# Kernel optimization log

Hardware: AMD Instinct MI355X
Metric: run time of the kernel (lower is better)

## Reference

```python
import jax, jax.numpy as jnp
import numpy as np

BN_EPS = 1e-5


def setup_inputs() -> dict:
    key = jax.random.key(0)
    k1, k2, k3, k4 = jax.random.split(key, 4)
    N, E, D_IN, D_OUT = 100000, 1600000, 128, 128
    x = jax.random.normal(k1, (N, D_IN), dtype=jnp.float32)
    edge_index = jax.random.randint(k2, (2, E), 0, N, dtype=jnp.int64)
    # GCNConv linear (glorot) + bias (zeros init in PyG)
    W = jax.random.normal(k3, (D_OUT, D_IN), dtype=jnp.float32) * (1.0 / np.sqrt(D_IN))
    b = jnp.zeros((D_OUT,), dtype=jnp.float32)
    # BatchNorm affine params
    gamma = jnp.ones((D_OUT,), dtype=jnp.float32)
    beta = jnp.zeros((D_OUT,), dtype=jnp.float32)
    return {"x": x, "edge_index": edge_index, "W": W, "b": b,
            "gamma": gamma, "beta": beta}


def reference(x, edge_index, W, b, gamma, beta):
    N = x.shape[0]
    # --- GCNConv: add self-loops, symmetric normalization ---
    loop = jnp.arange(N, dtype=edge_index.dtype)
    src = jnp.concatenate([edge_index[0], loop])  # [E+N]
    dst = jnp.concatenate([edge_index[1], loop])  # [E+N]
    deg = jax.ops.segment_sum(jnp.ones_like(dst, dtype=x.dtype), dst,
                              num_segments=N)  # in-degree incl. self-loop
    dinv = jnp.where(deg > 0, jax.lax.rsqrt(deg), 0.0)
    norm = dinv[src] * dinv[dst]  # [E+N]
    # linear transform before propagation (PyG GCNConv)
    h = x @ W.T  # [N, D_OUT]
    agg = jax.ops.segment_sum(h[src] * norm[:, None], dst, num_segments=N)
    out = agg + b
    # --- BatchNorm1d (training mode: batch statistics over nodes) ---
    mean = jnp.mean(out, axis=0)
    var = jnp.var(out, axis=0)
    out = (out - mean) * jax.lax.rsqrt(var + BN_EPS) * gamma + beta
    # --- ReLU, residual, dropout(p=0 -> identity) ---
    out = jax.nn.relu(out)
    out = out + x  # residual (in_dim == out_dim)
    return out
```

## Files before the change

### kernel.cpp

```cpp
#include <hip/hip_runtime.h>
#include <hip/hip_fp16.h>

#define BN_EPS 1e-5f

typedef unsigned int uint32;
typedef __attribute__((ext_vector_type(8))) _Float16 f16x8;
typedef __attribute__((ext_vector_type(4))) float f32x4;

union H2U { __half2 h; uint32 u; };

__device__ __forceinline__ __half2 u2h(uint32 u) { H2U c; c.u = u; return c.h; }
__device__ __forceinline__ uint32 h2u(__half2 h) { H2U c; c.h = h; return c.u; }
__device__ __forceinline__ uint32 pack2h(float a, float b) {
    return h2u(__halves2half2(__float2half_rn(a), __float2half_rn(b)));
}
__device__ __forceinline__ float h2lo(uint32 u) {
    return __half2float(__ushort_as_half((unsigned short)(u & 0xffffu)));
}
__device__ __forceinline__ float h2hi(uint32 u) {
    return __half2float(__ushort_as_half((unsigned short)(u >> 16)));
}


__global__ void __launch_bounds__(256) k_prep(const float4* __restrict__ x4, int nx4,
                                              const float4* __restrict__ w4, int nw4,
                                              const int* __restrict__ dst, int E, int NB,
                                              uint2* __restrict__ xh4, uint2* __restrict__ wh4,
                                              int* __restrict__ bcnt) {
    __shared__ int h[4][1024];
    int t = threadIdx.x;
    int wave = t >> 6;
    if (blockIdx.x < 256) {
        for (int i = t; i < 4 * 1024; i += 256) h[i >> 10][i & 1023] = 0;
        __syncthreads();
        int c0 = (int)((long long)blockIdx.x * E / 256);
        int c1 = (int)((long long)(blockIdx.x + 1) * E / 256);
        for (int e = c0 + t; e < c1; e += 256) atomicAdd(&h[wave][dst[e] >> 8], 1);
        __syncthreads();
        for (int i = t; i < NB; i += 256) {
            int s = h[0][i] + h[1][i] + h[2][i] + h[3][i];
            if (s) atomicAdd(&bcnt[i], s);
        }
    }
    int idx = blockIdx.x * 256 + t;
    int stride = gridDim.x * 256;
    for (int i = idx; i < nx4; i += stride) {
        float4 v = x4[i];
        xh4[i] = make_uint2(pack2h(v.x, v.y), pack2h(v.z, v.w));
    }
    for (int i = idx; i < nw4; i += stride) {
        float4 v = w4[i];
        wh4[i] = make_uint2(pack2h(v.x, v.y), pack2h(v.z, v.w));
    }
}


__global__ void k_scan1024(const int* __restrict__ in, int n, int* __restrict__ outExcl) {
    __shared__ int s[1024];
    int t = threadIdx.x;
    int v = (t < n) ? in[t] : 0;
    s[t] = v;
    __syncthreads();
    for (int off = 1; off < 1024; off <<= 1) {
        int add = (t >= off) ? s[t - off] : 0;
        __syncthreads();
        s[t] += add;
        __syncthreads();
    }
    if (t < n) outExcl[t] = s[t] - v;
    if (t == n - 1) outExcl[n] = s[t];
}


__global__ void __launch_bounds__(256) k_bscatter(const int* __restrict__ ei, int E, int NB,
                                                  const int* __restrict__ bbase,
                                                  int* __restrict__ bfill,
                                                  uint32* __restrict__ bpack) {
    __shared__ int h[4][1024];
    int t = threadIdx.x;
    int wave = t >> 6;
    int c0 = (int)((long long)blockIdx.x * E / gridDim.x);
    int c1 = (int)((long long)(blockIdx.x + 1) * E / gridDim.x);
    for (int i = t; i < 4 * 1024; i += 256) h[i >> 10][i & 1023] = 0;
    __syncthreads();
    for (int e = c0 + t; e < c1; e += 256)
        atomicAdd(&h[wave][ei[E + e] >> 8], 1);
    __syncthreads();
    for (int i = t; i < NB; i += 256) {
        int n0 = h[0][i], n1 = h[1][i], n2 = h[2][i], n3 = h[3][i];
        int tot = n0 + n1 + n2 + n3;
        if (tot > 0) {
            int base = bbase[i] + atomicAdd(&bfill[i], tot);
            h[0][i] = base;
            h[1][i] = base + n0;
            h[2][i] = base + n0 + n1;
            h[3][i] = base + n0 + n1 + n2;
        }
    }
    __syncthreads();
    for (int e = c0 + t; e < c1; e += 256) {
        int s = ei[e];
        int d = ei[E + e];
        int b = d >> 8;
        int pos = atomicAdd(&h[wave][b], 1);
        bpack[pos] = ((uint32)(d & 255) << 24) | (uint32)s;
    }
}


__global__ void __launch_bounds__(256) k_csr(const uint32* __restrict__ bpack,
                                             const int* __restrict__ bbase,
                                             int N, int E,
                                             int* __restrict__ rowptr,
                                             uint32* __restrict__ dpk,
                                             int* __restrict__ col) {
    __shared__ int h[4][256], s[256], cur[4][256];
    int b = blockIdx.x;
    int t = threadIdx.x;
    int wave = t >> 6;
    int e0 = bbase[b], e1 = bbase[b + 1];
    h[0][t] = 0; h[1][t] = 0; h[2][t] = 0; h[3][t] = 0;
    __syncthreads();
    for (int e = e0 + t; e < e1; e += 256)
        atomicAdd(&h[wave][bpack[e] >> 24], 1);
    __syncthreads();
    int n0 = h[0][t], n1 = h[1][t], n2 = h[2][t], n3 = h[3][t];
    int cnt = n0 + n1 + n2 + n3;
    s[t] = cnt;
    __syncthreads();
    for (int off = 1; off < 256; off <<= 1) {
        int add = (t >= off) ? s[t - off] : 0;
        __syncthreads();
        s[t] += add;
        __syncthreads();
    }
    int excl = s[t] - cnt;
    int node = (b << 8) + t;
    if (node < N) {
        rowptr[node] = e0 + excl;
        float dv = rsqrtf((float)(cnt + 1));
        dpk[node] = pack2h(dv, dv);
        if (node == N - 1) rowptr[N] = E;
    }
    cur[0][t] = e0 + excl;
    cur[1][t] = e0 + excl + n0;
    cur[2][t] = e0 + excl + n0 + n1;
    cur[3][t] = e0 + excl + n0 + n1 + n2;
    __syncthreads();
    for (int e = e0 + t; e < e1; e += 256) {
        uint32 p = bpack[e];
        int pos = atomicAdd(&cur[wave][p >> 24], 1);
        col[pos] = (int)(p & 0xffffffu);
    }
}


#define EDGE_FMA(vv, ww)                                   \
    acc0 = __hfma2(u2h((vv).x), u2h(ww), acc0);            \
    acc1 = __hfma2(u2h((vv).y), u2h(ww), acc1);            \
    acc2 = __hfma2(u2h((vv).z), u2h(ww), acc2);            \
    acc3 = __hfma2(u2h((vv).w), u2h(ww), acc3);

__global__ void __launch_bounds__(256) k_agg(const uint32* __restrict__ xh,
                                             const int* __restrict__ rowptr,
                                             const int* __restrict__ col,
                                             const uint32* __restrict__ dpk,
                                             uint32* __restrict__ aggh, int N) {
    int wid = blockIdx.x * 4 + (threadIdx.x >> 6);
    if (wid >= N) return;
    int lane = threadIdx.x & 63;
    int g = lane >> 4, c = lane & 15;

    __half2 z = __float2half2_rn(0.f);
    __half2 acc0 = z, acc1 = z, acc2 = z, acc3 = z;

    int e0 = rowptr[wid], e1 = rowptr[wid + 1];
    for (int cb = e0; cb < e1; cb += 64) {
        int rem = e1 - cb;
        int lim = rem < 64 ? rem : 64;
        int sL = (lane < lim) ? col[cb + lane] : 0;
        uint32 wL = (lane < lim) ? dpk[sL] : 0;
        int j0 = 0;
        for (; j0 + 16 <= lim; j0 += 16) {
            int jA = j0 + g, jB = j0 + 4 + g, jC = j0 + 8 + g, jD = j0 + 12 + g;
            int sA = __shfl(sL, jA), sB = __shfl(sL, jB);
            int sC = __shfl(sL, jC), sD = __shfl(sL, jD);
            uint32 wA = (uint32)__shfl((int)wL, jA), wB = (uint32)__shfl((int)wL, jB);
            uint32 wC = (uint32)__shfl((int)wL, jC), wD = (uint32)__shfl((int)wL, jD);
            uint4 vA = *(const uint4*)&xh[(size_t)sA * 64 + c * 4];
            uint4 vB = *(const uint4*)&xh[(size_t)sB * 64 + c * 4];
            uint4 vC = *(const uint4*)&xh[(size_t)sC * 64 + c * 4];
            uint4 vD = *(const uint4*)&xh[(size_t)sD * 64 + c * 4];
            EDGE_FMA(vA, wA); EDGE_FMA(vB, wB); EDGE_FMA(vC, wC); EDGE_FMA(vD, wD);
        }
        for (; j0 < lim; j0 += 4) {
            int j = j0 + g;
            int sj = __shfl(sL, j);
            uint32 wj = (uint32)__shfl((int)wL, j);
            uint4 v = *(const uint4*)&xh[(size_t)sj * 64 + c * 4];
            EDGE_FMA(v, wj);
        }
    }
    uint32 u;
    u = __shfl_xor(h2u(acc0), 16); acc0 = __hadd2(acc0, u2h(u));
    u = __shfl_xor(h2u(acc0), 32); acc0 = __hadd2(acc0, u2h(u));
    u = __shfl_xor(h2u(acc1), 16); acc1 = __hadd2(acc1, u2h(u));
    u = __shfl_xor(h2u(acc1), 32); acc1 = __hadd2(acc1, u2h(u));
    u = __shfl_xor(h2u(acc2), 16); acc2 = __hadd2(acc2, u2h(u));
    u = __shfl_xor(h2u(acc2), 32); acc2 = __hadd2(acc2, u2h(u));
    u = __shfl_xor(h2u(acc3), 16); acc3 = __hadd2(acc3, u2h(u));
    u = __shfl_xor(h2u(acc3), 32); acc3 = __hadd2(acc3, u2h(u));

    if (g == 0) {
        float di = h2lo(dpk[wid]);
        uint4 sv = *(const uint4*)&xh[(size_t)wid * 64 + c * 4];
        uint4 o;
        o.x = pack2h(di * (di * h2lo(sv.x) + __low2float(acc0)),
                     di * (di * h2hi(sv.x) + __high2float(acc0)));
        o.y = pack2h(di * (di * h2lo(sv.y) + __low2float(acc1)),
                     di * (di * h2hi(sv.y) + __high2float(acc1)));
        o.z = pack2h(di * (di * h2lo(sv.z) + __low2float(acc2)),
                     di * (di * h2hi(sv.z) + __high2float(acc2)));
        o.w = pack2h(di * (di * h2lo(sv.w) + __low2float(acc3)),
                     di * (di * h2hi(sv.w) + __high2float(acc3)));
        *(uint4*)&aggh[(size_t)wid * 64 + c * 4] = o;
    }
}


#define STAGE_W()                                                            \
    for (int m = threadIdx.x; m < 2048; m += 256) {                          \
        int row = m >> 4, cc = m & 15;                                       \
        uint4 v = *(const uint4*)&Wh[row * 128 + cc * 8];                    \
        *(uint4*)((char*)wlds + row * 256 + ((cc * 16) ^ ((row & 7) << 4))) = v; \
    }

#define MFMA_TILE(acc, tile)                                                 \
    {                                                                        \
        int arow = (tile) * 64 + wave * 16 + lrow;                           \
        bool avalid = arow < N;                                              \
        _Pragma("unroll")                                                    \
        for (int kc = 0; kc < 4; ++kc) {                                     \
            f16x8 a;                                                         \
            if (avalid) a = *(const f16x8*)&Ah[(size_t)arow * 128 + kc * 32 + g * 8]; \
            else        a = (f16x8){0, 0, 0, 0, 0, 0, 0, 0};                 \
            _Pragma("unroll")                                                \
            for (int ct = 0; ct < 8; ++ct) {                                 \
                int row = ct * 16 + lrow;                                    \
                const f16x8 bfr = *(const f16x8*)((const char*)wlds + row * 256 \
                                   + ((kc * 64 + g * 16) ^ ((row & 7) << 4))); \
                acc[ct] = __builtin_amdgcn_mfma_f32_16x16x32_f16(a, bfr, acc[ct], 0, 0, 0); \
            }                                                                \
        }                                                                    \
    }

__global__ void __launch_bounds__(256) k_gemm_stats(const _Float16* __restrict__ Ah,
                                                    const _Float16* __restrict__ Wh,
                                                    const float* __restrict__ bias,
                                                    int N, int ntiles,
                                                    float* __restrict__ partials) {
    __shared__ uint32 wlds[8192];
    __shared__ float red[1024];
    STAGE_W();
    __syncthreads();

    int t = threadIdx.x;
    int wave = t >> 6, lane = t & 63;
    int lrow = lane & 15, g = lane >> 4;

    float bv[8];
    #pragma unroll
    for (int ct = 0; ct < 8; ++ct) bv[ct] = bias[ct * 16 + lrow];

    float s[8], sq[8];
    #pragma unroll
    for (int ct = 0; ct < 8; ++ct) { s[ct] = 0.f; sq[ct] = 0.f; }

    for (int tile = blockIdx.x; tile < ntiles; tile += gridDim.x) {
        f32x4 acc[8];
        #pragma unroll
        for (int ct = 0; ct < 8; ++ct) acc[ct] = (f32x4){0.f, 0.f, 0.f, 0.f};
        MFMA_TILE(acc, tile);
        int orow0 = tile * 64 + wave * 16 + g * 4;
        #pragma unroll
        for (int ct = 0; ct < 8; ++ct) {
            #pragma unroll
            for (int rr = 0; rr < 4; ++rr) {
                if (orow0 + rr < N) {
                    float o = acc[ct][rr] + bv[ct];
                    s[ct] += o; sq[ct] += o * o;
                }
            }
        }
    }
    #pragma unroll
    for (int ct = 0; ct < 8; ++ct) {
        s[ct] += __shfl_xor(s[ct], 16); sq[ct] += __shfl_xor(sq[ct], 16);
        s[ct] += __shfl_xor(s[ct], 32); sq[ct] += __shfl_xor(sq[ct], 32);
    }
    if (lane < 16) {
        #pragma unroll
        for (int ct = 0; ct < 8; ++ct) {
            int colI = ct * 16 + lrow;
            red[wave * 256 + colI] = s[ct];
            red[wave * 256 + 128 + colI] = sq[ct];
        }
    }
    __syncthreads();
    if (t < 256)
        partials[blockIdx.x * 256 + t] = red[t] + red[256 + t] + red[512 + t] + red[768 + t];
}


__global__ void __launch_bounds__(1024) k_bnparams(const float* __restrict__ partials, int nblk,
                                                   const float* __restrict__ gamma,
                                                   const float* __restrict__ beta,
                                                   float invN, float* __restrict__ ss) {
    __shared__ float red[1024];
    int tid = threadIdx.x;
    int colI = tid & 255, q = tid >> 8;
    int bq = nblk >> 2;
    float v0 = 0.f, v1 = 0.f, v2 = 0.f, v3 = 0.f;
    int b0 = q * bq;
    for (int b = b0; b < b0 + bq; b += 4) {
        v0 += partials[(b + 0) * 256 + colI];
        v1 += partials[(b + 1) * 256 + colI];
        v2 += partials[(b + 2) * 256 + colI];
        v3 += partials[(b + 3) * 256 + colI];
    }
    red[q * 256 + colI] = (v0 + v1) + (v2 + v3);
    __syncthreads();
    if (tid < 256) {
        float tot = red[tid] + red[256 + tid] + red[512 + tid] + red[768 + tid];
        red[tid] = tot;
    }
    __syncthreads();
    if (tid < 128) {
        float mean = red[tid] * invN;
        float var = red[128 + tid] * invN - mean * mean;
        float sc = gamma[tid] * rsqrtf(var + BN_EPS);
        ss[tid] = sc;
        ss[128 + tid] = beta[tid] - mean * sc;
    }
}

__global__ void __launch_bounds__(256) k_gemm_apply(const _Float16* __restrict__ Ah,
                                                    const _Float16* __restrict__ Wh,
                                                    const float* __restrict__ bias,
                                                    const float* __restrict__ ss,
                                                    const uint32* __restrict__ xh,
                                                    int N, int ntiles,
                                                    float* __restrict__ out) {
    __shared__ uint32 wlds[8192];
    STAGE_W();
    __syncthreads();

    int t = threadIdx.x;
    int wave = t >> 6, lane = t & 63;
    int lrow = lane & 15, g = lane >> 4;

    float bv[8], scv[8], shv[8];
    #pragma unroll
    for (int ct = 0; ct < 8; ++ct) {
        int colI = ct * 16 + lrow;
        bv[ct] = bias[colI]; scv[ct] = ss[colI]; shv[ct] = ss[128 + colI];
    }

    for (int tile = blockIdx.x; tile < ntiles; tile += gridDim.x) {
        f32x4 acc[8];
        #pragma unroll
        for (int ct = 0; ct < 8; ++ct) acc[ct] = (f32x4){0.f, 0.f, 0.f, 0.f};
        MFMA_TILE(acc, tile);
        int orow0 = tile * 64 + wave * 16 + g * 4;
        #pragma unroll
        for (int ct = 0; ct < 8; ++ct) {
            int ocol = ct * 16 + lrow;
            #pragma unroll
            for (int rr = 0; rr < 4; ++rr) {
                int r = orow0 + rr;
                if (r < N) {
                    float pre = acc[ct][rr] + bv[ct];
                    float o = fmaxf(pre * scv[ct] + shv[ct], 0.f);
                    uint32 xv = xh[(size_t)r * 64 + (ocol >> 1)];
                    float xr = (ocol & 1) ? h2hi(xv) : h2lo(xv);
                    out[(size_t)r * 128 + ocol] = o + xr;
                }
            }
        }
    }
}


extern "C" void kernel_launch(void* const* d_in, const int* in_sizes, int n_in,
                              void* d_out, int out_size, void* d_ws, size_t ws_size,
                              hipStream_t stream) {
    const float* x     = (const float*)d_in[0];
    const int*   ei    = (const int*)d_in[1];
    const float* W     = (const float*)d_in[2];
    const float* bias  = (const float*)d_in[3];
    const float* gamma = (const float*)d_in[4];
    const float* beta  = (const float*)d_in[5];
    float* out = (float*)d_out;

    const int D = 128;
    int N = in_sizes[0] / D;
    int E = in_sizes[1] / 2;
    int NB = (N + 255) >> 8;

    const int GSTATS = 1024;
    const int GAPPLY = 1024;

    char* ws = (char*)d_ws;
    size_t off = 0;
    auto alloc = [&](size_t bytes) -> void* {
        void* p = ws + off;
        off += (bytes + 255) & ~(size_t)255;
        return p;
    };
    uint32* xh   = (uint32*)alloc((size_t)N * 64 * sizeof(uint32));
    uint32* aggh = (uint32*)alloc((size_t)N * 64 * sizeof(uint32));
    uint32* bpack= (uint32*)alloc((size_t)E * sizeof(uint32));
    int* col     = (int*)alloc((size_t)E * sizeof(int));
    _Float16* Wh = (_Float16*)alloc((size_t)D * D * sizeof(_Float16));
    int* rowptr  = (int*)alloc((size_t)(N + 1) * sizeof(int));
    uint32* dpk  = (uint32*)alloc((size_t)N * sizeof(uint32));
    int* bbase   = (int*)alloc(1025 * sizeof(int));
    float* ss    = (float*)alloc(256 * sizeof(float));
    float* partials = (float*)alloc((size_t)GSTATS * 256 * sizeof(float));
    int* bcnt    = (int*)alloc(1024 * sizeof(int));
    int* bfill   = (int*)alloc(1024 * sizeof(int));

    hipMemsetAsync(bcnt, 0, 2 * 1024 * sizeof(int), stream);

    k_prep<<<2048, 256, 0, stream>>>((const float4*)x, N * 32, (const float4*)W, D * D / 4,
                                     ei + E, E, NB, (uint2*)xh, (uint2*)Wh, bcnt);
    k_scan1024<<<1, 1024, 0, stream>>>(bcnt, NB, bbase);
    k_bscatter<<<256, 256, 0, stream>>>(ei, E, NB, bbase, bfill, bpack);
    k_csr<<<NB, 256, 0, stream>>>(bpack, bbase, N, E, rowptr, dpk, col);
    k_agg<<<(N + 3) / 4, 256, 0, stream>>>(xh, rowptr, col, dpk, aggh, N);

    int ntiles = (N + 63) / 64;
    k_gemm_stats<<<GSTATS, 256, 0, stream>>>((const _Float16*)aggh, Wh, bias, N, ntiles, partials);
    k_bnparams<<<1, 1024, 0, stream>>>(partials, GSTATS, gamma, beta, 1.0f / (float)N, ss);
    k_gemm_apply<<<GAPPLY, 256, 0, stream>>>((const _Float16*)aggh, Wh, bias, ss, xh, N, ntiles, out);
}
```

Measured before the change: 208.1 us.

## Replace bucket count+scan with fixed-capacity buckets and simplify edge gather loop

After: 181.1 us. 1.15x faster.

```diff
diff --git a/kernel.cpp b/kernel.cpp
--- a/kernel.cpp
+++ b/kernel.cpp
@@ -24,25 +24,8 @@
 
 __global__ void __launch_bounds__(256) k_prep(const float4* __restrict__ x4, int nx4,
                                               const float4* __restrict__ w4, int nw4,
-                                              const int* __restrict__ dst, int E, int NB,
-                                              uint2* __restrict__ xh4, uint2* __restrict__ wh4,
-                                              int* __restrict__ bcnt) {
-    __shared__ int h[4][1024];
-    int t = threadIdx.x;
-    int wave = t >> 6;
-    if (blockIdx.x < 256) {
-        for (int i = t; i < 4 * 1024; i += 256) h[i >> 10][i & 1023] = 0;
-        __syncthreads();
-        int c0 = (int)((long long)blockIdx.x * E / 256);
-        int c1 = (int)((long long)(blockIdx.x + 1) * E / 256);
-        for (int e = c0 + t; e < c1; e += 256) atomicAdd(&h[wave][dst[e] >> 8], 1);
-        __syncthreads();
-        for (int i = t; i < NB; i += 256) {
-            int s = h[0][i] + h[1][i] + h[2][i] + h[3][i];
-            if (s) atomicAdd(&bcnt[i], s);
-        }
-    }
-    int idx = blockIdx.x * 256 + t;
+                                              uint2* __restrict__ xh4, uint2* __restrict__ wh4) {
+    int idx = blockIdx.x * 256 + threadIdx.x;
     int stride = gridDim.x * 256;
     for (int i = idx; i < nx4; i += stride) {
         float4 v = x4[i];
@@ -55,26 +38,8 @@
 }
 
 
-__global__ void k_scan1024(const int* __restrict__ in, int n, int* __restrict__ outExcl) {
-    __shared__ int s[1024];
-    int t = threadIdx.x;
-    int v = (t < n) ? in[t] : 0;
-    s[t] = v;
-    __syncthreads();
-    for (int off = 1; off < 1024; off <<= 1) {
-        int add = (t >= off) ? s[t - off] : 0;
-        __syncthreads();
-        s[t] += add;
-        __syncthreads();
-    }
-    if (t < n) outExcl[t] = s[t] - v;
-    if (t == n - 1) outExcl[n] = s[t];
-}
-
-
 __global__ void __launch_bounds__(256) k_bscatter(const int* __restrict__ ei, int E, int NB,
-                                                  const int* __restrict__ bbase,
-                                                  int* __restrict__ bfill,
+                                                  int CAP, int* __restrict__ bfill,
                                                   uint32* __restrict__ bpack) {
     __shared__ int h[4][1024];
     int t = threadIdx.x;
@@ -90,7 +55,7 @@
         int n0 = h[0][i], n1 = h[1][i], n2 = h[2][i], n3 = h[3][i];
         int tot = n0 + n1 + n2 + n3;
         if (tot > 0) {
-            int base = bbase[i] + atomicAdd(&bfill[i], tot);
+            int base = i * CAP + atomicAdd(&bfill[i], tot);
             h[0][i] = base;
             h[1][i] = base + n0;
             h[2][i] = base + n0 + n1;
@@ -109,16 +74,17 @@
 
 
 __global__ void __launch_bounds__(256) k_csr(const uint32* __restrict__ bpack,
-                                             const int* __restrict__ bbase,
-                                             int N, int E,
+                                             const int* __restrict__ bfill, int CAP,
+                                             int N,
                                              int* __restrict__ rowptr,
+                                             int* __restrict__ rowcnt,
                                              uint32* __restrict__ dpk,
                                              int* __restrict__ col) {
     __shared__ int h[4][256], s[256], cur[4][256];
     int b = blockIdx.x;
     int t = threadIdx.x;
     int wave = t >> 6;
-    int e0 = bbase[b], e1 = bbase[b + 1];
+    int e0 = b * CAP, e1 = e0 + bfill[b];
     h[0][t] = 0; h[1][t] = 0; h[2][t] = 0; h[3][t] = 0;
     __syncthreads();
     for (int e = e0 + t; e < e1; e += 256)
@@ -138,9 +104,9 @@
     int node = (b << 8) + t;
     if (node < N) {
         rowptr[node] = e0 + excl;
+        rowcnt[node] = cnt;
         float dv = rsqrtf((float)(cnt + 1));
         dpk[node] = pack2h(dv, dv);
-        if (node == N - 1) rowptr[N] = E;
     }
     cur[0][t] = e0 + excl;
     cur[1][t] = e0 + excl + n0;
@@ -163,6 +129,7 @@
 
 __global__ void __launch_bounds__(256) k_agg(const uint32* __restrict__ xh,
                                              const int* __restrict__ rowptr,
+                                             const int* __restrict__ rowcnt,
                                              const int* __restrict__ col,
                                              const uint32* __restrict__ dpk,
                                              uint32* __restrict__ aggh, int N) {
@@ -174,32 +141,32 @@
     __half2 z = __float2half2_rn(0.f);
     __half2 acc0 = z, acc1 = z, acc2 = z, acc3 = z;
 
-    int e0 = rowptr[wid], e1 = rowptr[wid + 1];
-    for (int cb = e0; cb < e1; cb += 64) {
-        int rem = e1 - cb;
-        int lim = rem < 64 ? rem : 64;
-        int sL = (lane < lim) ? col[cb + lane] : 0;
-        uint32 wL = (lane < lim) ? dpk[sL] : 0;
-        int j0 = 0;
-        for (; j0 + 16 <= lim; j0 += 16) {
-            int jA = j0 + g, jB = j0 + 4 + g, jC = j0 + 8 + g, jD = j0 + 12 + g;
-            int sA = __shfl(sL, jA), sB = __shfl(sL, jB);
-            int sC = __shfl(sL, jC), sD = __shfl(sL, jD);
-            uint32 wA = (uint32)__shfl((int)wL, jA), wB = (uint32)__shfl((int)wL, jB);
-            uint32 wC = (uint32)__shfl((int)wL, jC), wD = (uint32)__shfl((int)wL, jD);
-            uint4 vA = *(const uint4*)&xh[(size_t)sA * 64 + c * 4];
-            uint4 vB = *(const uint4*)&xh[(size_t)sB * 64 + c * 4];
-            uint4 vC = *(const uint4*)&xh[(size_t)sC * 64 + c * 4];
-            uint4 vD = *(const uint4*)&xh[(size_t)sD * 64 + c * 4];
-            EDGE_FMA(vA, wA); EDGE_FMA(vB, wB); EDGE_FMA(vC, wC); EDGE_FMA(vD, wD);
-        }
-        for (; j0 < lim; j0 += 4) {
-            int j = j0 + g;
-            int sj = __shfl(sL, j);
-            uint32 wj = (uint32)__shfl((int)wL, j);
-            uint4 v = *(const uint4*)&xh[(size_t)sj * 64 + c * 4];
-            EDGE_FMA(v, wj);
-        }
+    int e0 = rowptr[wid];
+    int e1 = e0 + rowcnt[wid];
+    int e = e0;
+    for (; e + 16 <= e1; e += 16) {
+        int i0 = e + g, i1 = e + 4 + g, i2 = e + 8 + g, i3 = e + 12 + g;
+        int s0 = col[i0], s1 = col[i1], s2 = col[i2], s3 = col[i3];
+        uint32 w0 = dpk[s0], w1 = dpk[s1], w2 = dpk[s2], w3 = dpk[s3];
+        uint4 v0 = *(const uint4*)&xh[(size_t)s0 * 64 + c * 4];
+        uint4 v1 = *(const uint4*)&xh[(size_t)s1 * 64 + c * 4];
+        uint4 v2 = *(const uint4*)&xh[(size_t)s2 * 64 + c * 4];
+        uint4 v3 = *(const uint4*)&xh[(size_t)s3 * 64 + c * 4];
+        EDGE_FMA(v0, w0); EDGE_FMA(v1, w1); EDGE_FMA(v2, w2); EDGE_FMA(v3, w3);
+    }
+    if (e < e1) {
+        int i0 = e + g, i1 = e + 4 + g, i2 = e + 8 + g, i3 = e + 12 + g;
+        int s0 = 0, s1 = 0, s2 = 0, s3 = 0;
+        uint32 w0 = 0, w1 = 0, w2 = 0, w3 = 0;
+        if (i0 < e1) { s0 = col[i0]; w0 = dpk[s0]; }
+        if (i1 < e1) { s1 = col[i1]; w1 = dpk[s1]; }
+        if (i2 < e1) { s2 = col[i2]; w2 = dpk[s2]; }
+        if (i3 < e1) { s3 = col[i3]; w3 = dpk[s3]; }
+        uint4 v0 = *(const uint4*)&xh[(size_t)s0 * 64 + c * 4];
+        uint4 v1 = *(const uint4*)&xh[(size_t)s1 * 64 + c * 4];
+        uint4 v2 = *(const uint4*)&xh[(size_t)s2 * 64 + c * 4];
+        uint4 v3 = *(const uint4*)&xh[(size_t)s3 * 64 + c * 4];
+        EDGE_FMA(v0, w0); EDGE_FMA(v1, w1); EDGE_FMA(v2, w2); EDGE_FMA(v3, w3);
     }
     uint32 u;
     u = __shfl_xor(h2u(acc0), 16); acc0 = __hadd2(acc0, u2h(u));
@@ -406,9 +373,10 @@
     int N = in_sizes[0] / D;
     int E = in_sizes[1] / 2;
     int NB = (N + 255) >> 8;
-
-    const int GSTATS = 1024;
-    const int GAPPLY = 1024;
+    int CAP = ((E + NB - 1) / NB + 1024 + 63) & ~63;
+
+    const int GSTATS = 256;
+    const int GAPPLY = 512;
 
     char* ws = (char*)d_ws;
     size_t off = 0;
@@ -419,25 +387,23 @@
     };
     uint32* xh   = (uint32*)alloc((size_t)N * 64 * sizeof(uint32));
     uint32* aggh = (uint32*)alloc((size_t)N * 64 * sizeof(uint32));
-    uint32* bpack= (uint32*)alloc((size_t)E * sizeof(uint32));
-    int* col     = (int*)alloc((size_t)E * sizeof(int));
+    uint32* bpack= (uint32*)alloc((size_t)NB * CAP * sizeof(uint32));
+    int* col     = (int*)alloc((size_t)NB * CAP * sizeof(int));
     _Float16* Wh = (_Float16*)alloc((size_t)D * D * sizeof(_Float16));
-    int* rowptr  = (int*)alloc((size_t)(N + 1) * sizeof(int));
+    int* rowptr  = (int*)alloc((size_t)N * sizeof(int));
+    int* rowcnt  = (int*)alloc((size_t)N * sizeof(int));
     uint32* dpk  = (uint32*)alloc((size_t)N * sizeof(uint32));
-    int* bbase   = (int*)alloc(1025 * sizeof(int));
     float* ss    = (float*)alloc(256 * sizeof(float));
     float* partials = (float*)alloc((size_t)GSTATS * 256 * sizeof(float));
-    int* bcnt    = (int*)alloc(1024 * sizeof(int));
     int* bfill   = (int*)alloc(1024 * sizeof(int));
 
-    hipMemsetAsync(bcnt, 0, 2 * 1024 * sizeof(int), stream);
+    hipMemsetAsync(bfill, 0, 1024 * sizeof(int), stream);
 
     k_prep<<<2048, 256, 0, stream>>>((const float4*)x, N * 32, (const float4*)W, D * D / 4,
-                                     ei + E, E, NB, (uint2*)xh, (uint2*)Wh, bcnt);
-    k_scan1024<<<1, 1024, 0, stream>>>(bcnt, NB, bbase);
-    k_bscatter<<<256, 256, 0, stream>>>(ei, E, NB, bbase, bfill, bpack);
-    k_csr<<<NB, 256, 0, stream>>>(bpack, bbase, N, E, rowptr, dpk, col);
-    k_agg<<<(N + 3) / 4, 256, 0, stream>>>(xh, rowptr, col, dpk, aggh, N);
+                                     (uint2*)xh, (uint2*)Wh);
+    k_bscatter<<<256, 256, 0, stream>>>(ei, E, NB, CAP, bfill, bpack);
+    k_csr<<<NB, 256, 0, stream>>>(bpack, bfill, CAP, N, rowptr, rowcnt, dpk, col);
+    k_agg<<<(N + 3) / 4, 256, 0, stream>>>(xh, rowptr, rowcnt, col, dpk, aggh, N);
 
     int ntiles = (N + 63) / 64;
     k_gemm_stats<<<GSTATS, 256, 0, stream>>>((const _Float16*)aggh, Wh, bias, N, ntiles, partials);
```
